# Optimization experiments

Hardware: AMD Instinct MI355X
Metric: run time of the kernel (lower is better)

Reference implementation:

```python
import jax, jax.numpy as jnp
import numpy as np

D_MODEL = 256
EXPAND = 2
MAX_STEPS = 6
DILATIONS = (1, 2, 4)
EPS = 1e-6


def setup_inputs() -> dict:
    key = jax.random.key(0)
    ks = jax.random.split(key, 12)
    B, C, H, W = 8, D_MODEL, 64, 64
    d, dh = D_MODEL, D_MODEL * EXPAND
    init_logit = float(np.log(0.1 / (0.25 - 0.1 + 1e-08)))
    s = 1.0 / np.sqrt(d)
    return {
        "u": jax.random.normal(ks[0], (B, C, H, W), jnp.float32),
        "forcing": jax.random.normal(ks[1], (B, C, H, W), jnp.float32),
        "diff_logits": jnp.full((3, d), init_logit, jnp.float32),
        "w1": jax.random.uniform(ks[2], (d, dh), jnp.float32, -s, s),
        "b1": jax.random.uniform(ks[3], (dh,), jnp.float32, -s, s),
        "w2": jax.random.uniform(ks[4], (dh, d), jnp.float32, -1.0 / np.sqrt(dh), 1.0 / np.sqrt(dh)),
        "b2": jax.random.uniform(ks[5], (d,), jnp.float32, -1.0 / np.sqrt(dh), 1.0 / np.sqrt(dh)),
        "wf": jax.random.uniform(ks[6], (d, d), jnp.float32, -s, s),
        "bf": jax.random.uniform(ks[7], (d,), jnp.float32, -s, s),
        "wi": jax.random.uniform(ks[8], (d, d), jnp.float32, -s, s),
        "bi": jax.random.uniform(ks[9], (d,), jnp.float32, -s, s),
        "wc": jax.random.uniform(ks[10], (d, d), jnp.float32, -s, s),
        "bc": jax.random.uniform(ks[11], (d,), jnp.float32, -s, s),
        "norm_scale": jnp.ones((d,), jnp.float32),
        "log_dt": jnp.asarray(np.log(0.1), jnp.float32),
        "alpha_mem": jnp.asarray(0.1, jnp.float32),
        "alpha_force": jnp.asarray(0.1, jnp.float32),
    }


def _laplacian(u, diff_logits):
    # multi-dilation 5-point reflect-padded stencil, per-channel coeffs
    out = jnp.zeros_like(u)
    for i, d in enumerate(DILATIONS):
        coeff = 0.25 * jax.nn.sigmoid(diff_logits[i])  # (C,)
        p = jnp.pad(u, ((0, 0), (0, 0), (d, d), (d, d)), mode="reflect")
        lap = (p[:, :, d:-d, 2 * d:] + p[:, :, d:-d, :-2 * d]
               + p[:, :, 2 * d:, d:-d] + p[:, :, :-2 * d, d:-d] - 4.0 * u)
        out = out + coeff[None, :, None, None] * lap
    return out


def reference(u, forcing, diff_logits, w1, b1, w2, b2, wf, bf, wi, bi, wc, bc,
              norm_scale, log_dt, alpha_mem, alpha_force):
    B, C, H, W = u.shape
    dt = jnp.clip(jnp.exp(log_dt), 0.01, 0.3)
    h = jnp.zeros((B, C), u.dtype)
    inv_sqrt_c = 1.0 / float(np.sqrt(C))
    for t in range(MAX_STEPS):
        diff = _laplacian(u, diff_logits)
        # per-cell reaction MLP on channel axis (exact GELU, matching torch)
        hdn = jax.nn.gelu(jnp.einsum("bchw,ce->behw", u, w1) + b1[None, :, None, None],
                          approximate=False)
        react = jnp.einsum("behw,ec->bchw", hdn, w2) + b2[None, :, None, None]
        # gated global memory on pooled features
        pooled = u.mean(axis=(2, 3))  # (B, C)
        f = jax.nn.sigmoid(pooled @ wf + bf)
        i_ = jax.nn.sigmoid(pooled @ wi + bi)
        c = jnp.tanh(pooled @ wc + bc)
        h = h * f + i_ * c
        du = diff + react + alpha_mem * h[:, :, None, None] + alpha_force * forcing
        u = u + dt * du
        if (t + 1) % 2 == 0:
            # RMSNorm over channel dim
            rms = jnp.sqrt(jnp.sum(u * u, axis=1, keepdims=True)) * inv_sqrt_c
            u = u / (rms + EPS) * norm_scale[None, :, None, None]
    return u
```

## Files before the change

kernel.cpp:

```cpp
#include <hip/hip_runtime.h>
#include <math.h>

constexpr int NB = 8, NC = 256, NE = 512, NH = 64, NW = 64, NHW = NH * NW;
constexpr int STEPS = 6;

typedef short bfrag8 __attribute__((ext_vector_type(8)));
typedef float f32x4 __attribute__((ext_vector_type(4)));

__device__ __forceinline__ float sigm_(float x) { return 1.f / (1.f + expf(-x)); }
__device__ __forceinline__ float gelu_(float x) {
    return 0.5f * x * (1.f + erff(x * 0.70710678118654752f));
}
__device__ __forceinline__ ushort f2bf(float f) {
    unsigned u = __builtin_bit_cast(unsigned, f);
    unsigned r = (u + 0x7fffu + ((u >> 16) & 1u)) >> 16;
    return (ushort)r;
}
__device__ __forceinline__ float bf2f(ushort us) {
    return __builtin_bit_cast(float, (unsigned)us << 16);
}
__device__ __forceinline__ void gload16(const void* g, void* l) {
    __builtin_amdgcn_global_load_lds((const __attribute__((address_space(1))) void*)g,
                                     (__attribute__((address_space(3))) void*)l, 16, 0, 0);
}

__global__ void wt_kernel(const float* __restrict__ w1, const float* __restrict__ w2,
                          ushort* __restrict__ w1t, ushort* __restrict__ w2t) {
    const int bid = blockIdx.x, tid = threadIdx.x;
    if (bid < NE) {
        w1t[bid * NC + tid] = f2bf(w1[(size_t)tid * NE + bid]);
    } else {
        const int c = bid - NE;
        for (int e = tid; e < NE; e += 256)
            w2t[c * NE + e] = f2bf(w2[(size_t)e * NC + c]);
    }
}

__global__ void fconv_kernel(const float* __restrict__ fin, ushort* __restrict__ fout) {
    const size_t i8 = ((size_t)blockIdx.x * 256 + threadIdx.x) * 8;
    const float4 a = *reinterpret_cast<const float4*>(fin + i8);
    const float4 b = *reinterpret_cast<const float4*>(fin + i8 + 4);
    uint4 o;
    o.x = (unsigned)f2bf(a.x) | ((unsigned)f2bf(a.y) << 16);
    o.y = (unsigned)f2bf(a.z) | ((unsigned)f2bf(a.w) << 16);
    o.z = (unsigned)f2bf(b.x) | ((unsigned)f2bf(b.y) << 16);
    o.w = (unsigned)f2bf(b.z) | ((unsigned)f2bf(b.w) << 16);
    *reinterpret_cast<uint4*>(fout + i8) = o;
}

__global__ __launch_bounds__(256) void x0_kernel(const float* __restrict__ u,
                                                 ushort* __restrict__ X,
                                                 float* __restrict__ rowsums) {
    __shared__ ushort xs[64][264];
    const int tid = threadIdx.x;
    const int b = blockIdx.x >> 6, y = blockIdx.x & 63;
    const float* up = u + (size_t)b * NC * NHW + y * NW;
#pragma unroll
    for (int cc = 0; cc < 4; ++cc)
#pragma unroll
        for (int i = 0; i < 16; ++i) {
            const int idx = i * 256 + tid;
            const int c = idx >> 6, x = idx & 63;
            xs[x][cc * 64 + c] = f2bf(up[(size_t)(cc * 64 + c) * NHW + x]);
        }
    __syncthreads();
    ushort* Xp = X + ((size_t)b * NHW + y * NW) * NC;
    const int wv = tid >> 6, lane = tid & 63;
#pragma unroll
    for (int r = 0; r < 16; ++r) {
        const int row = wv * 16 + r;
        *reinterpret_cast<uint2*>(Xp + (size_t)row * NC + lane * 4) =
            *reinterpret_cast<const uint2*>(&xs[row][lane * 4]);
    }
    const float* rp = up + (size_t)tid * NHW;
    float s = 0.f;
#pragma unroll
    for (int x = 0; x < 64; ++x) s += rp[x];
    rowsums[((size_t)b * 64 + y) * NC + tid] = s;
}

__global__ void h_kernel(const float* __restrict__ rowsums,
                         const float* __restrict__ wf, const float* __restrict__ bfv,
                         const float* __restrict__ wi, const float* __restrict__ biv,
                         const float* __restrict__ wc, const float* __restrict__ bcv,
                         float* __restrict__ h, const int first) {
    const int b = blockIdx.x;
    const int c = threadIdx.x;
    __shared__ float sp[NC];
    const float* rs = rowsums + (size_t)b * 64 * NC + c;
    float s = 0.f;
#pragma unroll
    for (int y = 0; y < 64; ++y) s += rs[y * NC];
    sp[c] = s * (1.f / 4096.f);
    __syncthreads();
    float af = bfv[c], ai = biv[c], ac = bcv[c];
    for (int k = 0; k < NC; ++k) {
        const float p = sp[k];
        af = fmaf(p, wf[k * NC + c], af);
        ai = fmaf(p, wi[k * NC + c], ai);
        ac = fmaf(p, wc[k * NC + c], ac);
    }
    const float f  = sigm_(af);
    const float ii = sigm_(ai);
    const float cc = tanhf(ac);
    const float hold = first ? 0.f : h[b * NC + c];
    h[b * NC + c] = hold * f + ii * cc;
}

__global__ __launch_bounds__(256, 2) void step_kernel(
    const ushort* __restrict__ Xg, const ushort* __restrict__ w1t,
    const ushort* __restrict__ w2t, const float* __restrict__ b1,
    const float* __restrict__ b2, const float* __restrict__ uin,
    const ushort* __restrict__ forc, const float* __restrict__ dlog,
    const float* __restrict__ hbuf, const float* __restrict__ nsc,
    const float* __restrict__ p_logdt, const float* __restrict__ p_am,
    const float* __restrict__ p_af, const int do_norm,
    float* __restrict__ uout, ushort* __restrict__ Xout,
    float* __restrict__ rowsums) {
    __shared__ __align__(16) char pool[73728];
    ushort* Xs = (ushort*)pool;
    ushort* Wb = (ushort*)(pool + 32768);
    ushort* Hs = (ushort*)(pool + 65536);

    const int tid = threadIdx.x;
    const int wv = tid >> 6, lane = tid & 63;
    const int r16 = lane & 15, kg = lane >> 4;
    const int work = (blockIdx.x & 7) * 64 + (blockIdx.x >> 3);
    const int b = work >> 6, y = work & 63;
    const int m0 = work * 64;

#pragma unroll
    for (int i = 0; i < 8; ++i) {
        const int idx = i * 256 + tid, row = idx >> 5, s = idx & 31;
        gload16(Xg + (size_t)(m0 + row) * NC + ((s ^ (row & 7)) << 3), Xs + idx * 8);
    }

    f32x4 acc2[4][4];
#pragma unroll
    for (int ct = 0; ct < 4; ++ct)
#pragma unroll
        for (int p = 0; p < 4; ++p) acc2[ct][p] = (f32x4){0.f, 0.f, 0.f, 0.f};

    for (int ec = 0; ec < 8; ++ec) {
        __syncthreads();
#pragma unroll
        for (int i = 0; i < 8; ++i) {
            const int idx = i * 256 + tid, row = idx >> 5, s = idx & 31;
            gload16(w1t + (size_t)(ec * 64 + row) * NC + ((s ^ (row & 7)) << 3),
                    Wb + idx * 8);
        }
        __syncthreads();
        f32x4 acc1[4];
#pragma unroll
        for (int p = 0; p < 4; ++p) acc1[p] = (f32x4){0.f, 0.f, 0.f, 0.f};
#pragma unroll
        for (int kk = 0; kk < 8; ++kk) {
            const int g = kk * 4 + kg;
            const int ra = wv * 16 + r16;
            const bfrag8 a = *(const bfrag8*)(Wb + ra * 256 + ((g ^ (ra & 7)) << 3));
#pragma unroll
            for (int p = 0; p < 4; ++p) {
                const int rb = p * 16 + r16;
                const bfrag8 bb = *(const bfrag8*)(Xs + rb * 256 + ((g ^ (rb & 7)) << 3));
                acc1[p] = __builtin_amdgcn_mfma_f32_16x16x32_bf16(a, bb, acc1[p], 0, 0, 0);
            }
        }
        __syncthreads();
        const float4 b1v = *(const float4*)(b1 + ec * 64 + wv * 16 + kg * 4);
        const float bj[4] = {b1v.x, b1v.y, b1v.z, b1v.w};
#pragma unroll
        for (int p = 0; p < 4; ++p) {
            ushort4 hv;
            hv.x = f2bf(gelu_(acc1[p][0] + bj[0]));
            hv.y = f2bf(gelu_(acc1[p][1] + bj[1]));
            hv.z = f2bf(gelu_(acc1[p][2] + bj[2]));
            hv.w = f2bf(gelu_(acc1[p][3] + bj[3]));
            const int px = p * 16 + r16;
            const int gH = wv * 2 + (kg >> 1);
            *(ushort4*)(Hs + px * 64 + ((gH ^ (px & 7)) << 3) + ((kg & 1) << 2)) = hv;
        }
#pragma unroll
        for (int i = 0; i < 8; ++i) {
            const int idx = i * 256 + tid, row = idx >> 3, s = idx & 7;
            gload16(w2t + (size_t)row * NE + ec * 64 + ((s ^ (row & 7)) << 3),
                    Wb + idx * 8);
        }
        __syncthreads();
#pragma unroll
        for (int kk = 0; kk < 2; ++kk) {
            const int g = kk * 4 + kg;
            bfrag8 bfr[4];
#pragma unroll
            for (int p = 0; p < 4; ++p) {
                const int rb = p * 16 + r16;
                bfr[p] = *(const bfrag8*)(Hs + rb * 64 + ((g ^ (rb & 7)) << 3));
            }
#pragma unroll
            for (int ct = 0; ct < 4; ++ct) {
                const int ra = wv * 64 + ct * 16 + r16;
                const bfrag8 a = *(const bfrag8*)(Wb + ra * 64 + ((g ^ (ra & 7)) << 3));
#pragma unroll
                for (int p = 0; p < 4; ++p)
                    acc2[ct][p] = __builtin_amdgcn_mfma_f32_16x16x32_bf16(a, bfr[p],
                                                                          acc2[ct][p], 0, 0, 0);
            }
        }
    }

    float* trh = (float*)pool;
    float* su  = (float*)(pool + 34816);
    const int eg = tid >> 4, pg = tid & 15, x0p = pg * 4;
    const float dt = fminf(fmaxf(expf(p_logdt[0]), 0.01f), 0.3f);
    const float am = p_am[0], afc = p_af[0];
    const float* ub = uin + (size_t)b * NC * NHW;
    const ushort* frow = forc + (size_t)b * NC * NHW + (size_t)y * NW;

    float unew[4][4][4];

#pragma unroll
    for (int h2 = 0; h2 < 2; ++h2) {
        __syncthreads();
        if ((wv >> 1) == h2) {
#pragma unroll
            for (int ct = 0; ct < 4; ++ct)
#pragma unroll
                for (int p = 0; p < 4; ++p)
#pragma unroll
                    for (int j = 0; j < 4; ++j)
                        trh[((wv & 1) * 64 + ct * 16 + kg * 4 + j) * 68 + p * 16 + r16] =
                            acc2[ct][p][j];
        }
#pragma unroll
        for (int chi = 0; chi < 2; ++chi) {
            const int ch = h2 * 2 + chi;
            __syncthreads();
#pragma unroll
            for (int i = 0; i < 16; ++i) {
                const int idx = i * 256 + tid;
                const int r = idx >> 6, q = idx & 63;
                su[r * 68 + q] = ub[(size_t)(ch * 64 + r) * NHW + (size_t)y * NW + q];
            }
            __syncthreads();
#pragma unroll
            for (int jc = 0; jc < 4; ++jc) {
                const int cc = eg * 4 + jc;
                const int c = ch * 64 + cc;
                const float co0 = 0.25f * sigm_(dlog[c]);
                const float co1 = 0.25f * sigm_(dlog[NC + c]);
                const float co2 = 0.25f * sigm_(dlog[2 * NC + c]);
                const float hterm = am * hbuf[b * NC + c];
                const float b2v = b2[c];
                const float* up = ub + (size_t)c * NHW;

                float ym[6][4];
                const int dy[6] = {-1, 1, -2, 2, -4, 4};
#pragma unroll
                for (int n = 0; n < 6; ++n) {
                    int ry = y + dy[n];
                    ry = ry < 0 ? -ry : (ry > 63 ? 126 - ry : ry);
                    const float4 t = *reinterpret_cast<const float4*>(up + (size_t)ry * NW + x0p);
                    ym[n][0] = t.x; ym[n][1] = t.y; ym[n][2] = t.z; ym[n][3] = t.w;
                }
                const uint2 fr = *reinterpret_cast<const uint2*>(frow + (size_t)c * NHW + x0p);
                float fv[4];
                fv[0] = bf2f((ushort)(fr.x & 0xffff));
                fv[1] = bf2f((ushort)(fr.x >> 16));
                fv[2] = bf2f((ushort)(fr.y & 0xffff));
                fv[3] = bf2f((ushort)(fr.y >> 16));
                const f32x4 rv = *reinterpret_cast<const f32x4*>(&trh[(chi * 64 + cc) * 68 + x0p]);
#pragma unroll
                for (int ip = 0; ip < 4; ++ip) {
                    const int x = x0p + ip;
                    const float uc = su[cc * 68 + x];
                    int xm, xp2;
                    float dsum = 0.f, lap;
                    xm = x - 1; xm = xm < 0 ? -xm : xm;
                    xp2 = x + 1; xp2 = xp2 > 63 ? 126 - xp2 : xp2;
                    lap = su[cc * 68 + xm] + su[cc * 68 + xp2] + ym[0][ip] + ym[1][ip] - 4.f * uc;
                    dsum = fmaf(co0, lap, dsum);
                    xm = x - 2; xm = xm < 0 ? -xm : xm;
                    xp2 = x + 2; xp2 = xp2 > 63 ? 126 - xp2 : xp2;
                    lap = su[cc * 68 + xm] + su[cc * 68 + xp2] + ym[2][ip] + ym[3][ip] - 4.f * uc;
                    dsum = fmaf(co1, lap, dsum);
                    xm = x - 4; xm = xm < 0 ? -xm : xm;
                    xp2 = x + 4; xp2 = xp2 > 63 ? 126 - xp2 : xp2;
                    lap = su[cc * 68 + xm] + su[cc * 68 + xp2] + ym[4][ip] + ym[5][ip] - 4.f * uc;
                    dsum = fmaf(co2, lap, dsum);

                    const float du_ = dsum + rv[ip] + b2v + hterm + afc * fv[ip];
                    unew[ch][jc][ip] = uc + dt * du_;
                }
            }
        }
    }

    float* redc = (float*)(pool + 34816);
    float* inv64p = (float*)(pool + 39168);
    if (do_norm) {
        float ps[4] = {0.f, 0.f, 0.f, 0.f};
#pragma unroll
        for (int ch = 0; ch < 4; ++ch)
#pragma unroll
            for (int jc = 0; jc < 4; ++jc)
#pragma unroll
                for (int ip = 0; ip < 4; ++ip)
                    ps[ip] = fmaf(unew[ch][jc][ip], unew[ch][jc][ip], ps[ip]);
        __syncthreads();
        *reinterpret_cast<f32x4*>(&redc[eg * 68 + x0p]) = (f32x4){ps[0], ps[1], ps[2], ps[3]};
        __syncthreads();
        if (tid < 64) {
            float s = 0.f;
#pragma unroll
            for (int g = 0; g < 16; ++g) s += redc[g * 68 + tid];
            inv64p[tid] = 1.f / (sqrtf(s) * 0.0625f + 1e-6f);
        }
    }
    __syncthreads();

    ushort* xs = (ushort*)pool;
    float* sums = (float*)(pool + 36864);
    float persum[4][4];
    float* uob = uout + (size_t)b * NC * NHW + (size_t)y * NW;
#pragma unroll
    for (int ch = 0; ch < 4; ++ch)
#pragma unroll
        for (int jc = 0; jc < 4; ++jc) {
            const int cc = eg * 4 + jc;
            const int c = ch * 64 + cc;
            const float ns = do_norm ? nsc[c] : 1.f;
            float vv[4];
#pragma unroll
            for (int ip = 0; ip < 4; ++ip) {
                float v = unew[ch][jc][ip];
                if (do_norm) v *= inv64p[x0p + ip] * ns;
                vv[ip] = v;
                xs[(x0p + ip) * 264 + c] = f2bf(v);
            }
            persum[ch][jc] = vv[0] + vv[1] + vv[2] + vv[3];
            float4 o; o.x = vv[0]; o.y = vv[1]; o.z = vv[2]; o.w = vv[3];
            *reinterpret_cast<float4*>(uob + (size_t)c * NHW + x0p) = o;
        }
    __syncthreads();
#pragma unroll
    for (int ch = 0; ch < 4; ++ch)
#pragma unroll
        for (int jc = 0; jc < 4; ++jc)
            sums[(ch * 64 + eg * 4 + jc) * 16 + pg] = persum[ch][jc];
    ushort* Xp = Xout + (size_t)m0 * NC;
#pragma unroll
    for (int r = 0; r < 16; ++r) {
        const int row = wv * 16 + r;
        *reinterpret_cast<uint2*>(Xp + (size_t)row * NC + lane * 4) =
            *reinterpret_cast<const uint2*>(&xs[row * 264 + lane * 4]);
    }
    __syncthreads();
    {
        float s = 0.f;
#pragma unroll
        for (int g = 0; g < 16; ++g) s += sums[tid * 16 + g];
        rowsums[((size_t)b * 64 + y) * NC + tid] = s;
    }
}

extern "C" void kernel_launch(void* const* d_in, const int* in_sizes, int n_in,
                              void* d_out, int out_size, void* d_ws, size_t ws_size,
                              hipStream_t stream) {
    (void)in_sizes; (void)n_in; (void)out_size; (void)ws_size;
    const float* u0      = (const float*)d_in[0];
    const float* forcing = (const float*)d_in[1];
    const float* dlog    = (const float*)d_in[2];
    const float* w1      = (const float*)d_in[3];
    const float* b1      = (const float*)d_in[4];
    const float* w2      = (const float*)d_in[5];
    const float* b2      = (const float*)d_in[6];
    const float* wf      = (const float*)d_in[7];
    const float* bfv     = (const float*)d_in[8];
    const float* wi      = (const float*)d_in[9];
    const float* biv     = (const float*)d_in[10];
    const float* wc      = (const float*)d_in[11];
    const float* bcv     = (const float*)d_in[12];
    const float* nsc     = (const float*)d_in[13];
    const float* p_logdt = (const float*)d_in[14];
    const float* p_am    = (const float*)d_in[15];
    const float* p_af    = (const float*)d_in[16];

    float* uout = (float*)d_out;

    char* w = (char*)d_ws;
    float*  uA     = (float*)w;   w += (size_t)NB * NC * NHW * 4;
    ushort* X      = (ushort*)w;  w += (size_t)NB * NHW * NC * 2;
    ushort* forc   = (ushort*)w;  w += (size_t)NB * NC * NHW * 2;
    ushort* w1t    = (ushort*)w;  w += (size_t)NE * NC * 2;
    ushort* w2t    = (ushort*)w;  w += (size_t)NC * NE * 2;
    float* rowsums = (float*)w;   w += (size_t)NB * NH * NC * 4;
    float* hbuf    = (float*)w;   w += (size_t)NB * NC * 4;

    wt_kernel<<<768, 256, 0, stream>>>(w1, w2, w1t, w2t);
    fconv_kernel<<<4096, 256, 0, stream>>>(forcing, forc);
    x0_kernel<<<NB * NH, 256, 0, stream>>>(u0, X, rowsums);

    const float* src = u0;
    for (int t = 0; t < STEPS; ++t) {
        float* dst = (t & 1) ? uout : uA;
        h_kernel<<<NB, 256, 0, stream>>>(rowsums, wf, bfv, wi, biv, wc, bcv, hbuf, t == 0);
        step_kernel<<<NB * NH, 256, 0, stream>>>(X, w1t, w2t, b1, b2, src, forc, dlog,
                                                 hbuf, nsc, p_logdt, p_am, p_af,
                                                 ((t + 1) % 2) == 0, dst, X, rowsums);
        src = dst;
    }
}
```

Baseline: 624.9 us.

## Keep MLP weight fragments in registers, double-buffer hidden tile, parallelize gate kernel

The step kernel now loads W1 and W2 MFMA fragments straight from global memory into registers, prefetching the next W1 chunk. This replaces the shared-memory staging of weights and removes several barriers per chunk. The hidden-activation tile is double-buffered, the shared pool shrinks (which may allow more blocks per CU), the u reload is vectorised to float4, the bf16 X output is written directly without a shared transpose, and the sums array is padded to avoid bank conflicts. The gates kernel uses 768 threads so the three gate matvecs and the row-sum reduction run in parallel. Costs are higher register pressure and uncoalesced global fragment reads that depend on L2 hits.

```diff
diff --git a/kernel.cpp b/kernel.cpp
--- a/kernel.cpp
+++ b/kernel.cpp
@@ -79,32 +79,40 @@
     rowsums[((size_t)b * 64 + y) * NC + tid] = s;
 }
 
-__global__ void h_kernel(const float* __restrict__ rowsums,
-                         const float* __restrict__ wf, const float* __restrict__ bfv,
-                         const float* __restrict__ wi, const float* __restrict__ biv,
-                         const float* __restrict__ wc, const float* __restrict__ bcv,
-                         float* __restrict__ h, const int first) {
+__global__ __launch_bounds__(768) void gates_kernel(
+    const float* __restrict__ rowsums,
+    const float* __restrict__ wf, const float* __restrict__ bfv,
+    const float* __restrict__ wi, const float* __restrict__ biv,
+    const float* __restrict__ wc, const float* __restrict__ bcv,
+    float* __restrict__ h, const int first) {
     const int b = blockIdx.x;
-    const int c = threadIdx.x;
-    __shared__ float sp[NC];
+    const int tid = threadIdx.x;
+    const int g = tid >> 8, c = tid & 255;
+    __shared__ float sp[256];
+    __shared__ float psum[3][256];
+    __shared__ float gf[256], gi[256];
+    const int y0 = (g == 0) ? 0 : (g == 1) ? 21 : 42;
+    const int y1 = (g == 0) ? 21 : (g == 1) ? 42 : 64;
     const float* rs = rowsums + (size_t)b * 64 * NC + c;
     float s = 0.f;
-#pragma unroll
-    for (int y = 0; y < 64; ++y) s += rs[y * NC];
-    sp[c] = s * (1.f / 4096.f);
-    __syncthreads();
-    float af = bfv[c], ai = biv[c], ac = bcv[c];
-    for (int k = 0; k < NC; ++k) {
-        const float p = sp[k];
-        af = fmaf(p, wf[k * NC + c], af);
-        ai = fmaf(p, wi[k * NC + c], ai);
-        ac = fmaf(p, wc[k * NC + c], ac);
-    }
-    const float f  = sigm_(af);
-    const float ii = sigm_(ai);
-    const float cc = tanhf(ac);
-    const float hold = first ? 0.f : h[b * NC + c];
-    h[b * NC + c] = hold * f + ii * cc;
+    for (int y = y0; y < y1; ++y) s += rs[y * NC];
+    psum[g][c] = s;
+    __syncthreads();
+    if (g == 0) sp[c] = (psum[0][c] + psum[1][c] + psum[2][c]) * (1.f / 4096.f);
+    __syncthreads();
+    const float* W  = (g == 0) ? wf  : (g == 1) ? wi  : wc;
+    const float* Bv = (g == 0) ? bfv : (g == 1) ? biv : bcv;
+    float a = Bv[c];
+#pragma unroll 8
+    for (int k = 0; k < 256; ++k) a = fmaf(sp[k], W[k * NC + c], a);
+    if (g == 0) gf[c] = sigm_(a);
+    else if (g == 1) gi[c] = sigm_(a);
+    __syncthreads();
+    if (g == 2) {
+        const float cc = tanhf(a);
+        const float hold = first ? 0.f : h[b * NC + c];
+        h[b * NC + c] = hold * gf[c] + gi[c] * cc;
+    }
 }
 
 __global__ __launch_bounds__(256, 2) void step_kernel(
@@ -117,10 +125,8 @@
     const float* __restrict__ p_af, const int do_norm,
     float* __restrict__ uout, ushort* __restrict__ Xout,
     float* __restrict__ rowsums) {
-    __shared__ __align__(16) char pool[73728];
+    __shared__ __align__(16) char pool[52224];
     ushort* Xs = (ushort*)pool;
-    ushort* Wb = (ushort*)(pool + 32768);
-    ushort* Hs = (ushort*)(pool + 65536);
 
     const int tid = threadIdx.x;
     const int wv = tid >> 6, lane = tid & 63;
@@ -135,37 +141,47 @@
         gload16(Xg + (size_t)(m0 + row) * NC + ((s ^ (row & 7)) << 3), Xs + idx * 8);
     }
 
+    const ushort* w1base = w1t + (size_t)(wv * 16 + r16) * NC + kg * 8;
+    bfrag8 w1f[8], w2f[8];
+#pragma unroll
+    for (int kk = 0; kk < 8; ++kk)
+        w1f[kk] = *(const bfrag8*)(w1base + kk * 32);
+
     f32x4 acc2[4][4];
 #pragma unroll
     for (int ct = 0; ct < 4; ++ct)
 #pragma unroll
         for (int p = 0; p < 4; ++p) acc2[ct][p] = (f32x4){0.f, 0.f, 0.f, 0.f};
 
+    __syncthreads();
+
     for (int ec = 0; ec < 8; ++ec) {
-        __syncthreads();
-#pragma unroll
-        for (int i = 0; i < 8; ++i) {
-            const int idx = i * 256 + tid, row = idx >> 5, s = idx & 31;
-            gload16(w1t + (size_t)(ec * 64 + row) * NC + ((s ^ (row & 7)) << 3),
-                    Wb + idx * 8);
-        }
-        __syncthreads();
+#pragma unroll
+        for (int ct = 0; ct < 4; ++ct)
+#pragma unroll
+            for (int kk = 0; kk < 2; ++kk)
+                w2f[ct * 2 + kk] = *(const bfrag8*)(w2t
+                    + (size_t)(wv * 64 + ct * 16 + r16) * NE + ec * 64 + (kk * 4 + kg) * 8);
+
         f32x4 acc1[4];
 #pragma unroll
         for (int p = 0; p < 4; ++p) acc1[p] = (f32x4){0.f, 0.f, 0.f, 0.f};
 #pragma unroll
         for (int kk = 0; kk < 8; ++kk) {
             const int g = kk * 4 + kg;
-            const int ra = wv * 16 + r16;
-            const bfrag8 a = *(const bfrag8*)(Wb + ra * 256 + ((g ^ (ra & 7)) << 3));
 #pragma unroll
             for (int p = 0; p < 4; ++p) {
                 const int rb = p * 16 + r16;
                 const bfrag8 bb = *(const bfrag8*)(Xs + rb * 256 + ((g ^ (rb & 7)) << 3));
-                acc1[p] = __builtin_amdgcn_mfma_f32_16x16x32_bf16(a, bb, acc1[p], 0, 0, 0);
+                acc1[p] = __builtin_amdgcn_mfma_f32_16x16x32_bf16(w1f[kk], bb, acc1[p], 0, 0, 0);
             }
         }
-        __syncthreads();
+        if (ec < 7) {
+#pragma unroll
+            for (int kk = 0; kk < 8; ++kk)
+                w1f[kk] = *(const bfrag8*)(w1base + (size_t)(ec + 1) * 64 * NC + kk * 32);
+        }
+        ushort* Hs = (ushort*)(pool + 32768 + (ec & 1) * 8192);
         const float4 b1v = *(const float4*)(b1 + ec * 64 + wv * 16 + kg * 4);
         const float bj[4] = {b1v.x, b1v.y, b1v.z, b1v.w};
 #pragma unroll
@@ -179,12 +195,6 @@
             const int gH = wv * 2 + (kg >> 1);
             *(ushort4*)(Hs + px * 64 + ((gH ^ (px & 7)) << 3) + ((kg & 1) << 2)) = hv;
         }
-#pragma unroll
-        for (int i = 0; i < 8; ++i) {
-            const int idx = i * 256 + tid, row = idx >> 3, s = idx & 7;
-            gload16(w2t + (size_t)row * NE + ec * 64 + ((s ^ (row & 7)) << 3),
-                    Wb + idx * 8);
-        }
         __syncthreads();
 #pragma unroll
         for (int kk = 0; kk < 2; ++kk) {
@@ -196,14 +206,11 @@
                 bfr[p] = *(const bfrag8*)(Hs + rb * 64 + ((g ^ (rb & 7)) << 3));
             }
 #pragma unroll
-            for (int ct = 0; ct < 4; ++ct) {
-                const int ra = wv * 64 + ct * 16 + r16;
-                const bfrag8 a = *(const bfrag8*)(Wb + ra * 64 + ((g ^ (ra & 7)) << 3));
+            for (int ct = 0; ct < 4; ++ct)
 #pragma unroll
                 for (int p = 0; p < 4; ++p)
-                    acc2[ct][p] = __builtin_amdgcn_mfma_f32_16x16x32_bf16(a, bfr[p],
-                                                                          acc2[ct][p], 0, 0, 0);
-            }
+                    acc2[ct][p] = __builtin_amdgcn_mfma_f32_16x16x32_bf16(w2f[ct * 2 + kk],
+                                                                          bfr[p], acc2[ct][p], 0, 0, 0);
         }
     }
 
@@ -235,10 +242,11 @@
             const int ch = h2 * 2 + chi;
             __syncthreads();
 #pragma unroll
-            for (int i = 0; i < 16; ++i) {
+            for (int i = 0; i < 4; ++i) {
                 const int idx = i * 256 + tid;
-                const int r = idx >> 6, q = idx & 63;
-                su[r * 68 + q] = ub[(size_t)(ch * 64 + r) * NHW + (size_t)y * NW + q];
+                const int r = idx >> 4, q = (idx & 15) * 4;
+                *(float4*)&su[r * 68 + q] =
+                    *(const float4*)(ub + (size_t)(ch * 64 + r) * NHW + (size_t)y * NW + q);
             }
             __syncthreads();
 #pragma unroll
@@ -295,7 +303,7 @@
     }
 
     float* redc = (float*)(pool + 34816);
-    float* inv64p = (float*)(pool + 39168);
+    float* inv64p = (float*)pool;
     if (do_norm) {
         float ps[4] = {0.f, 0.f, 0.f, 0.f};
 #pragma unroll
@@ -317,47 +325,47 @@
     }
     __syncthreads();
 
-    ushort* xs = (ushort*)pool;
-    float* sums = (float*)(pool + 36864);
+    float* sums = (float*)(pool + 34816);
     float persum[4][4];
     float* uob = uout + (size_t)b * NC * NHW + (size_t)y * NW;
 #pragma unroll
-    for (int ch = 0; ch < 4; ++ch)
+    for (int ch = 0; ch < 4; ++ch) {
+        float vsc[4][4];
 #pragma unroll
         for (int jc = 0; jc < 4; ++jc) {
             const int cc = eg * 4 + jc;
             const int c = ch * 64 + cc;
             const float ns = do_norm ? nsc[c] : 1.f;
-            float vv[4];
 #pragma unroll
             for (int ip = 0; ip < 4; ++ip) {
                 float v = unew[ch][jc][ip];
                 if (do_norm) v *= inv64p[x0p + ip] * ns;
-                vv[ip] = v;
-                xs[(x0p + ip) * 264 + c] = f2bf(v);
+                vsc[jc][ip] = v;
             }
-            persum[ch][jc] = vv[0] + vv[1] + vv[2] + vv[3];
-            float4 o; o.x = vv[0]; o.y = vv[1]; o.z = vv[2]; o.w = vv[3];
+            persum[ch][jc] = vsc[jc][0] + vsc[jc][1] + vsc[jc][2] + vsc[jc][3];
+            float4 o; o.x = vsc[jc][0]; o.y = vsc[jc][1]; o.z = vsc[jc][2]; o.w = vsc[jc][3];
             *reinterpret_cast<float4*>(uob + (size_t)c * NHW + x0p) = o;
         }
-    __syncthreads();
+#pragma unroll
+        for (int ip = 0; ip < 4; ++ip) {
+            ushort4 xv;
+            xv.x = f2bf(vsc[0][ip]);
+            xv.y = f2bf(vsc[1][ip]);
+            xv.z = f2bf(vsc[2][ip]);
+            xv.w = f2bf(vsc[3][ip]);
+            *reinterpret_cast<ushort4*>(Xout + (size_t)(m0 + x0p + ip) * NC + ch * 64 + eg * 4) = xv;
+        }
+    }
 #pragma unroll
     for (int ch = 0; ch < 4; ++ch)
 #pragma unroll
         for (int jc = 0; jc < 4; ++jc)
-            sums[(ch * 64 + eg * 4 + jc) * 16 + pg] = persum[ch][jc];
-    ushort* Xp = Xout + (size_t)m0 * NC;
-#pragma unroll
-    for (int r = 0; r < 16; ++r) {
-        const int row = wv * 16 + r;
-        *reinterpret_cast<uint2*>(Xp + (size_t)row * NC + lane * 4) =
-            *reinterpret_cast<const uint2*>(&xs[row * 264 + lane * 4]);
-    }
+            sums[(ch * 64 + eg * 4 + jc) * 17 + pg] = persum[ch][jc];
     __syncthreads();
     {
         float s = 0.f;
 #pragma unroll
-        for (int g = 0; g < 16; ++g) s += sums[tid * 16 + g];
+        for (int g = 0; g < 16; ++g) s += sums[tid * 17 + g];
         rowsums[((size_t)b * 64 + y) * NC + tid] = s;
     }
 }
@@ -402,7 +410,7 @@
     const float* src = u0;
     for (int t = 0; t < STEPS; ++t) {
         float* dst = (t & 1) ? uout : uA;
-        h_kernel<<<NB, 256, 0, stream>>>(rowsums, wf, bfv, wi, biv, wc, bcv, hbuf, t == 0);
+        gates_kernel<<<NB, 768, 0, stream>>>(rowsums, wf, bfv, wi, biv, wc, bcv, hbuf, t == 0);
         step_kernel<<<NB * NH, 256, 0, stream>>>(X, w1t, w2t, b1, b2, src, forc, dlog,
                                                  hbuf, nsc, p_logdt, p_am, p_af,
                                                  ((t + 1) % 2) == 0, dst, X, rowsums);
```

Result: slower. 733.9 us (+17.4%).
